# Optimization experiments

Measured on AMD Instinct MI355X. Metric: run time of the kernel, lower is better.

## Reference

```python
import jax, jax.numpy as jnp
import numpy as np

# ---- instant-NGP hash-grid config (matches module hparams) ----
L = 16              # num_levels
F = 2               # n_feats per level (hard-coded in lotd_auto_compute_cfg)
T = 2 ** 19         # log2_hashmap_size = 19
BASE, DESIRED = 16, 2048
N = 2097152         # ray samples per batch
GEO = 15            # geo_feat_dim
HID = 64            # layer_dim
APP_N, APP_D = 1000, 48
SH_DIM = 16         # degree-4 spherical harmonics

_b = np.exp(np.log(DESIRED / BASE) / (L - 1))
RES = jnp.asarray(np.floor(BASE * _b ** np.arange(L)).astype(np.float32))
OFFS = jnp.asarray(np.array([[(i >> 2) & 1, (i >> 1) & 1, i & 1] for i in range(8)]), jnp.uint32)
PRIMES = jnp.array([1, 2654435761, 805459861], dtype=jnp.uint32)


def hash_encode(x01, table):
    """x01: [N,3] in [0,1]; table: [L,T,F] -> [N, L*F] multi-res hash features."""
    def level(res, emb):
        xs = x01 * res                      # [N,3]
        x0 = jnp.floor(xs)
        w = xs - x0                         # trilinear weights
        c = x0.astype(jnp.uint32)[:, None, :] + OFFS[None]          # [N,8,3] corners
        h = c * PRIMES[None, None, :]       # uint32 wrap-around multiply
        idx = (h[..., 0] ^ h[..., 1] ^ h[..., 2]) & jnp.uint32(T - 1)  # [N,8] spatial hash
        f = emb[idx]                        # [N,8,F] gather
        ws = jnp.prod(jnp.where(OFFS[None] == 1, w[:, None, :], 1.0 - w[:, None, :]), axis=-1)
        return jnp.einsum('nc,ncf->nf', ws, f)
    feats = jax.vmap(level, in_axes=(0, 0), out_axes=1)(RES, table)  # [N,L,F]
    return feats.reshape(x01.shape[0], L * F)


def sh16(d):
    """degree-4 real spherical harmonics of unit dirs d: [N,3] -> [N,16]."""
    x, y, z = d[:, 0], d[:, 1], d[:, 2]
    xx, yy, zz = x * x, y * y, z * z
    xy, yz, xz = x * y, y * z, x * z
    return jnp.stack([
        0.28209479177387814 * jnp.ones_like(x),
        -0.48860251190291987 * y, 0.48860251190291987 * z, -0.48860251190291987 * x,
        1.0925484305920792 * xy, -1.0925484305920792 * yz,
        0.94617469575755997 * zz - 0.31539156525252005,
        -1.0925484305920792 * xz, 0.54627421529603959 * (xx - yy),
        -0.59004358992664352 * y * (3.0 * xx - yy),
        2.8906114426405538 * xy * z,
        -0.45704579946446572 * y * (4.0 * zz - xx - yy),
        0.37317633259011546 * z * (2.0 * zz - 3.0 * xx - 3.0 * yy),
        -0.45704579946446572 * x * (4.0 * zz - xx - yy),
        1.4453057213202769 * z * (xx - yy),
        -0.59004358992664352 * x * (xx - 3.0 * yy),
    ], axis=-1)


def setup_inputs() -> dict:
    key = jax.random.key(0)
    ks = jax.random.split(key, 16)
    def w(k, i, o):
        return jax.random.normal(k, (i, o), jnp.float32) / np.sqrt(i)
    x = jax.random.uniform(ks[0], (N, 3), jnp.float32, -1.0, 1.0)   # points in [-1,1]^3
    d = jax.random.normal(ks[1], (N, 3), jnp.float32)
    app_idx = jax.random.randint(ks[2], (N,), 0, APP_N, jnp.int32)
    hash_table = jax.random.uniform(ks[3], (L, T, F), jnp.float32, -1e-4, 1e-4)
    app_table = jax.random.normal(ks[4], (APP_N, APP_D), jnp.float32) * 0.05
    ci = GEO + SH_DIM + APP_D
    return {
        'x': x, 'd': d, 'app_idx': app_idx,
        'hash_table': hash_table, 'app_table': app_table,
        'sw0': w(ks[5], L * F, HID), 'sb0': jnp.zeros((HID,), jnp.float32),
        'sw1': w(ks[6], HID, 1 + GEO), 'sb1': jnp.zeros((1 + GEO,), jnp.float32),
        'cw0': w(ks[7], ci, HID), 'cb0': jnp.zeros((HID,), jnp.float32),
        'cw1': w(ks[8], HID, HID), 'cb1': jnp.zeros((HID,), jnp.float32),
        'cw2': w(ks[9], HID, 3), 'cb2': jnp.zeros((3,), jnp.float32),
    }


def reference(x, d, app_idx, hash_table, app_table,
              sw0, sb0, sw1, sb1, cw0, cb0, cw1, cb1, cw2, cb2):
    x01 = (x + 1.0) * 0.5                      # normalize to [0,1]^3
    enc = hash_encode(x01, hash_table)          # [N, 32]
    h = jax.nn.relu(enc @ sw0 + sb0)
    h = h @ sw1 + sb1                           # [N, 1+GEO]
    sigma = jax.nn.softplus(100.0 * h[:, :1]) / 100.0   # softplus(beta=100)
    geo = h[:, 1:]
    dn = d / jnp.linalg.norm(d, axis=-1, keepdims=True)
    sh = sh16(dn)                               # [N,16]
    a = app_table[app_idx]                      # [N,48] appearance embedding
    c = jnp.concatenate([geo, sh, a], axis=-1)
    c = jax.nn.relu(c @ cw0 + cb0)
    c = jax.nn.relu(c @ cw1 + cb1)
    rgb = jax.nn.sigmoid(c @ cw2 + cb2)         # [N,3]
    return jnp.concatenate([sigma, rgb], axis=-1)   # [N,4]
```

## Files before the change

### kernel.cpp

```cpp
#include <hip/hip_runtime.h>
#include <cmath>
#include <type_traits>

#define NL 16
#define TBL_N (1u << 19)
#define HID 64
#define NDL 6

typedef float f4v __attribute__((ext_vector_type(4)));
typedef float f2v __attribute__((ext_vector_type(2)));
typedef short s8v __attribute__((ext_vector_type(8)));
typedef unsigned int u32;
typedef unsigned short u16;

struct Res16 { float r[NL]; };
struct DenseP { int R[NDL]; int off[NDL]; int total; };

__device__ __host__ __forceinline__ unsigned short f2bf(float f) {
    unsigned u = __builtin_bit_cast(unsigned, f);
    unsigned r = (u + 0x7FFFu + ((u >> 16) & 1u)) >> 16;
    return (unsigned short)r;
}
__device__ __forceinline__ u32 pack_bf(float a, float b) {
    return (u32)f2bf(a) | ((u32)f2bf(b) << 16);
}
__device__ __forceinline__ void corner_vals(unsigned v, float& f0, float& f1) {
    f0 = __uint_as_float(v << 16);
    f1 = __uint_as_float(v & 0xffff0000u);
}
__device__ __forceinline__ void corner_vals(float2 v, float& f0, float& f1) {
    f0 = v.x; f1 = v.y;
}

__global__ __launch_bounds__(256) void repack_bf16(const float* __restrict__ src,
                                                   unsigned* __restrict__ dst, int n) {
    int i = blockIdx.x * blockDim.x + threadIdx.x;
    if (i >= n) return;
    f2v v = __builtin_nontemporal_load((const f2v*)src + i);
    dst[i] = pack_bf(v.x, v.y);
}

__global__ __launch_bounds__(256) void pos_prep(
    const float* __restrict__ x, f4v* __restrict__ pos, int p0, int P, int n_pts)
{
    int p = blockIdx.x * 256 + threadIdx.x;
    if (p >= P) return;
    int n = p0 + p;
    f4v v;
    v.x = (__builtin_nontemporal_load(&x[3*n+0]) + 1.f) * 0.5f;
    v.y = (__builtin_nontemporal_load(&x[3*n+1]) + 1.f) * 0.5f;
    v.z = (__builtin_nontemporal_load(&x[3*n+2]) + 1.f) * 0.5f;
    v.w = 0.f;
    pos[p] = v;
}

__global__ __launch_bounds__(256) void build_dense4(
    const u32* __restrict__ tbl, uint4* __restrict__ dense, DenseP dp)
{
    int e = blockIdx.x * 256 + threadIdx.x;
    if (e >= dp.total) return;
    int l = 0;
    #pragma unroll
    for (int i = 1; i < NDL; i++) if (e >= dp.off[i]) l = i;
    int cell = e - dp.off[l];
    int R = dp.R[l];
    int Z = cell % R; int t = cell / R; int Y = t % R; int X = t / R;
    u32 hy0 = (u32)Y * 2654435761u, hy1 = hy0 + 2654435761u;
    u32 hz0 = (u32)Z * 805459861u,  hz1 = hz0 + 805459861u;
    const u32* base = tbl + (size_t)l * TBL_N;
    uint4 v;
    v.x = base[((u32)X ^ hy0 ^ hz0) & (TBL_N - 1u)];
    v.y = base[((u32)X ^ hy0 ^ hz1) & (TBL_N - 1u)];
    v.z = base[((u32)X ^ hy1 ^ hz0) & (TBL_N - 1u)];
    v.w = base[((u32)X ^ hy1 ^ hz1) & (TBL_N - 1u)];
    dense[e] = v;
}

__global__ __launch_bounds__(256) void nerf_encode(
    const f4v* __restrict__ pos,
    const uint2* __restrict__ tbl2,
    const uint4* __restrict__ dense,
    u32* __restrict__ enc,
    Res16 rt, DenseP dp, int P)
{
    int l = blockIdx.y;
    int tid = threadIdx.x;
    int p = blockIdx.x * 256 + tid;
    int pc = min(p, P - 1);

    f4v pv = pos[pc];
    float px = pv.x, py = pv.y, pz = pv.z;

    float res = rt.r[l];
    float xs = px*res, ys = py*res, zs = pz*res;
    float fx = floorf(xs), fy = floorf(ys), fz = floorf(zs);
    float wx = xs - fx, wy = ys - fy, wz = zs - fz;
    float ax = 1.f - wx, ay = 1.f - wy, az = 1.f - wz;

    float e0 = 0.f, e1 = 0.f;
    if (l < NDL) {
        int R = dp.R[l];
        int X = (int)fx, Y = (int)fy, Z = (int)fz;
        const uint4* dl = dense + dp.off[l];
        int c00 = (X * R + Y) * R + Z;
        uint4 v0 = dl[c00];
        uint4 v1 = dl[c00 + R * R];
        float s00 = ay*az, s01 = ay*wz, s10 = wy*az, s11 = wy*wz;
        float f0, f1;
        corner_vals(v0.x, f0, f1); e0 += ax*s00*f0; e1 += ax*s00*f1;
        corner_vals(v0.y, f0, f1); e0 += ax*s01*f0; e1 += ax*s01*f1;
        corner_vals(v0.z, f0, f1); e0 += ax*s10*f0; e1 += ax*s10*f1;
        corner_vals(v0.w, f0, f1); e0 += ax*s11*f0; e1 += ax*s11*f1;
        corner_vals(v1.x, f0, f1); e0 += wx*s00*f0; e1 += wx*s00*f1;
        corner_vals(v1.y, f0, f1); e0 += wx*s01*f0; e1 += wx*s01*f1;
        corner_vals(v1.z, f0, f1); e0 += wx*s10*f0; e1 += wx*s10*f1;
        corner_vals(v1.w, f0, f1); e0 += wx*s11*f0; e1 += wx*s11*f1;
    } else {
        unsigned X = (unsigned)fx;
        unsigned Y = (unsigned)fy, Z = (unsigned)fz;
        unsigned hy0 = Y * 2654435761u, hy1 = hy0 + 2654435761u;
        unsigned hz0 = Z * 805459861u,  hz1 = hz0 + 805459861u;
        bool xodd = (X & 1u) != 0u;
        const uint2* b2 = tbl2 + (size_t)l * (TBL_N / 2);
        #pragma unroll
        for (int c = 0; c < 4; c++) {
            unsigned hyz = ((c & 2) ? hy1 : hy0) ^ ((c & 1) ? hz1 : hz0);
            float wyz = ((c & 2) ? wy : ay) * ((c & 1) ? wz : az);
            unsigned idxA = (X ^ hyz) & (TBL_N - 1u);
            uint2 vA = b2[idxA >> 1];
            u32 a = (idxA & 1u) ? vA.y : vA.x;
            u32 b = (idxA & 1u) ? vA.x : vA.y;
            if (xodd) {
                unsigned idxB = ((X + 1u) ^ hyz) & (TBL_N - 1u);
                uint2 vB = b2[idxB >> 1];
                b = (idxB & 1u) ? vB.y : vB.x;
            }
            float fa0, fa1, fb0, fb1;
            corner_vals(a, fa0, fa1);
            corner_vals(b, fb0, fb1);
            e0 += wyz * (ax * fa0 + wx * fb0);
            e1 += wyz * (ax * fa1 + wx * fb1);
        }
    }
    __builtin_nontemporal_store(pack_bf(e0, e1), &enc[(size_t)l * P + pc]);
}

__global__ __launch_bounds__(256) void nerf_pack_w(
    const float* __restrict__ sw0, const float* __restrict__ sb0,
    const float* __restrict__ sw1, const float* __restrict__ sb1,
    const float* __restrict__ cw0, const float* __restrict__ cb0,
    const float* __restrict__ cw1, const float* __restrict__ cb1,
    const float* __restrict__ cw2, const float* __restrict__ cb2,
    u16* __restrict__ wf, float* __restrict__ bi)
{
    int tid = threadIdx.x;
    for (int e = tid; e < 14336; e += 256) {
        int f = e >> 9, r = e & 511, lane = r >> 3, j = r & 7;
        int fo = lane & 15, G = lane >> 4;
        float val = 0.f;
        if (f < 4) {
            int o = f*16 + fo, i = G*8 + j;
            val = sw0[i*64 + o];
        } else if (f < 6) {
            int o = fo, i = (f-4)*32 + G*8 + j;
            val = sw1[i*16 + o];
        } else if (f < 18) {
            int t = f - 6, mt = t / 3, kt = t % 3;
            int o = mt*16 + fo, i = kt*32 + G*8 + j;
            int row = (i < 16) ? (15 + i) : (i < 64) ? (31 + (i - 16)) : (i < 79) ? (i - 64) : -1;
            val = (row < 0) ? 0.f : cw0[row*64 + o];
        } else if (f < 26) {
            int t = f - 18, mt = t >> 1, kt = t & 1;
            int o = mt*16 + fo, i = kt*32 + G*8 + j;
            val = cw1[i*64 + o];
        } else {
            int kt = f - 26;
            int o = fo, i = kt*32 + G*8 + j;
            val = (o < 3) ? cw2[i*3 + o] : 0.f;
        }
        wf[e] = f2bf(val);
    }
    for (int i2 = tid; i2 < 224; i2 += 256) {
        float v;
        if (i2 < 64) v = sb0[i2];
        else if (i2 < 80) v = sb1[i2 - 64];
        else if (i2 < 144) v = cb0[i2 - 80];
        else if (i2 < 208) v = cb1[i2 - 144];
        else v = (i2 - 208 < 3) ? cb2[i2 - 208] : 0.f;
        bi[i2] = v;
    }
}

#define ASTRIDE 104

__global__ __launch_bounds__(256) void nerf_mlp_mfma(
    const u16* __restrict__ wfg, const float* __restrict__ big,
    const u32* __restrict__ enc,
    const float* __restrict__ dvec, const int* __restrict__ app_idx,
    const float* __restrict__ app_table,
    float* __restrict__ out, int p0, int P, int n_pts)
{
    __shared__ __align__(16) u16 WF[14336];
    __shared__ __align__(16) float BI[224];
    __shared__ __align__(16) u16 ACT[4][16 * ASTRIDE];

    int tid = threadIdx.x;
    int w = tid >> 6, l = tid & 63;
    int G = l >> 4, pq = l & 15;

    for (int i = tid; i < 1792; i += 256) ((uint4*)WF)[i] = ((const uint4*)wfg)[i];
    for (int i = tid; i < 224; i += 256) BI[i] = big[i];
    if (G == 3) {
        ACT[w][pq*ASTRIDE + 79] = 0;
        #pragma unroll
        for (int k = 0; k < 8; k++) *(u32*)&ACT[w][pq*ASTRIDE + 80 + 2*k] = 0u;
    }
    __syncthreads();

    #pragma unroll 1
    for (int g = 0; g < 4; g++) {
        int pl = blockIdx.x * 256 + w * 64 + g * 16 + pq;
        int pc = min(pl, P - 1);
        int n = p0 + pc;

        uint4 ed;
        {
            const u32* encp = enc + pc;
            ed.x = __builtin_nontemporal_load(encp + (size_t)(4*G+0) * P);
            ed.y = __builtin_nontemporal_load(encp + (size_t)(4*G+1) * P);
            ed.z = __builtin_nontemporal_load(encp + (size_t)(4*G+2) * P);
            ed.w = __builtin_nontemporal_load(encp + (size_t)(4*G+3) * P);
        }
        s8v encf = __builtin_bit_cast(s8v, ed);
        float dx = __builtin_nontemporal_load(&dvec[3*n+0]);
        float dy = __builtin_nontemporal_load(&dvec[3*n+1]);
        float dz = __builtin_nontemporal_load(&dvec[3*n+2]);
        int ai = app_idx[n];
        const f4v* arow = (const f4v*)(app_table + (size_t)ai * 48 + 12 * G);
        f4v a0 = arow[0], a1 = arow[1], a2 = arow[2];

        f4v acc0[4];
        #pragma unroll
        for (int mt = 0; mt < 4; mt++) acc0[mt] = *(const f4v*)&BI[mt*16 + 4*G];
        #pragma unroll
        for (int mt = 0; mt < 4; mt++) {
            s8v wfr = *(const s8v*)&WF[mt*512 + l*8];
            acc0[mt] = __builtin_amdgcn_mfma_f32_16x16x32_bf16(wfr, encf, acc0[mt], 0, 0, 0);
        }
        #pragma unroll
        for (int mt = 0; mt < 4; mt++) {
            f4v v = acc0[mt];
            *(u32*)&ACT[w][pq*ASTRIDE + mt*16 + 4*G]     = pack_bf(fmaxf(v[0],0.f), fmaxf(v[1],0.f));
            *(u32*)&ACT[w][pq*ASTRIDE + mt*16 + 4*G + 2] = pack_bf(fmaxf(v[2],0.f), fmaxf(v[3],0.f));
        }

        f4v acc1 = *(const f4v*)&BI[64 + 4*G];
        #pragma unroll
        for (int kt = 0; kt < 2; kt++) {
            s8v b = *(const s8v*)&ACT[w][pq*ASTRIDE + kt*32 + G*8];
            s8v wfr = *(const s8v*)&WF[(4+kt)*512 + l*8];
            acc1 = __builtin_amdgcn_mfma_f32_16x16x32_bf16(wfr, b, acc1, 0, 0, 0);
        }
        float sig_raw = acc1[0];

        {
            float invn = 1.0f / sqrtf(dx*dx + dy*dy + dz*dz);
            float ndx = dx*invn, ndy = dy*invn, ndz = dz*invn;
            float xx = ndx*ndx, yy = ndy*ndy, zz = ndz*ndz;
            float xy = ndx*ndy, yz = ndy*ndz, xz = ndx*ndz;
            float s0, s1, s2, s3;
            if (G == 0) {
                s0 =  0.28209479177387814f;
                s1 = -0.48860251190291987f * ndy;
                s2 =  0.48860251190291987f * ndz;
                s3 = -0.48860251190291987f * ndx;
            } else if (G == 1) {
                s0 =  1.0925484305920792f * xy;
                s1 = -1.0925484305920792f * yz;
                s2 =  0.94617469575756f * zz - 0.31539156525252005f;
                s3 = -1.0925484305920792f * xz;
            } else if (G == 2) {
                s0 =  0.5462742152960396f * (xx - yy);
                s1 = -0.5900435899266435f * ndy * (3.f*xx - yy);
                s2 =  2.890611442640554f * xy * ndz;
                s3 = -0.4570457994644657f * ndy * (4.f*zz - xx - yy);
            } else {
                s0 =  0.37317633259011546f * ndz * (2.f*zz - 3.f*xx - 3.f*yy);
                s1 = -0.4570457994644657f * ndx * (4.f*zz - xx - yy);
                s2 =  1.445305721320277f * ndz * (xx - yy);
                s3 = -0.5900435899266435f * ndx * (xx - 3.f*yy);
            }
            *(u32*)&ACT[w][pq*ASTRIDE + 4*G]     = pack_bf(s0, s1);
            *(u32*)&ACT[w][pq*ASTRIDE + 4*G + 2] = pack_bf(s2, s3);
            *(u32*)&ACT[w][pq*ASTRIDE + 16 + 12*G     ] = pack_bf(a0[0], a0[1]);
            *(u32*)&ACT[w][pq*ASTRIDE + 16 + 12*G + 2 ] = pack_bf(a0[2], a0[3]);
            *(u32*)&ACT[w][pq*ASTRIDE + 16 + 12*G + 4 ] = pack_bf(a1[0], a1[1]);
            *(u32*)&ACT[w][pq*ASTRIDE + 16 + 12*G + 6 ] = pack_bf(a1[2], a1[3]);
            *(u32*)&ACT[w][pq*ASTRIDE + 16 + 12*G + 8 ] = pack_bf(a2[0], a2[1]);
            *(u32*)&ACT[w][pq*ASTRIDE + 16 + 12*G + 10] = pack_bf(a2[2], a2[3]);
            #pragma unroll
            for (int r2 = 0; r2 < 4; r2++) {
                int fp = 4*G + r2;
                if (fp >= 1) ACT[w][pq*ASTRIDE + 63 + fp] = f2bf(acc1[r2]);
            }
        }

        f4v acc[4];
        #pragma unroll
        for (int mt = 0; mt < 4; mt++) acc[mt] = *(const f4v*)&BI[80 + mt*16 + 4*G];
        #pragma unroll
        for (int kt = 0; kt < 3; kt++) {
            s8v b = *(const s8v*)&ACT[w][pq*ASTRIDE + kt*32 + G*8];
            #pragma unroll
            for (int mt = 0; mt < 4; mt++) {
                s8v wfr = *(const s8v*)&WF[(6 + mt*3 + kt)*512 + l*8];
                acc[mt] = __builtin_amdgcn_mfma_f32_16x16x32_bf16(wfr, b, acc[mt], 0, 0, 0);
            }
        }
        #pragma unroll
        for (int mt = 0; mt < 4; mt++) {
            f4v v = acc[mt];
            *(u32*)&ACT[w][pq*ASTRIDE + mt*16 + 4*G]     = pack_bf(fmaxf(v[0],0.f), fmaxf(v[1],0.f));
            *(u32*)&ACT[w][pq*ASTRIDE + mt*16 + 4*G + 2] = pack_bf(fmaxf(v[2],0.f), fmaxf(v[3],0.f));
        }

        #pragma unroll
        for (int mt = 0; mt < 4; mt++) acc[mt] = *(const f4v*)&BI[144 + mt*16 + 4*G];
        #pragma unroll
        for (int kt = 0; kt < 2; kt++) {
            s8v b = *(const s8v*)&ACT[w][pq*ASTRIDE + kt*32 + G*8];
            #pragma unroll
            for (int mt = 0; mt < 4; mt++) {
                s8v wfr = *(const s8v*)&WF[(18 + mt*2 + kt)*512 + l*8];
                acc[mt] = __builtin_amdgcn_mfma_f32_16x16x32_bf16(wfr, b, acc[mt], 0, 0, 0);
            }
        }
        #pragma unroll
        for (int mt = 0; mt < 4; mt++) {
            f4v v = acc[mt];
            *(u32*)&ACT[w][pq*ASTRIDE + mt*16 + 4*G]     = pack_bf(fmaxf(v[0],0.f), fmaxf(v[1],0.f));
            *(u32*)&ACT[w][pq*ASTRIDE + mt*16 + 4*G + 2] = pack_bf(fmaxf(v[2],0.f), fmaxf(v[3],0.f));
        }

        f4v acc2 = *(const f4v*)&BI[208 + 4*G];
        #pragma unroll
        for (int kt = 0; kt < 2; kt++) {
            s8v b = *(const s8v*)&ACT[w][pq*ASTRIDE + kt*32 + G*8];
            s8v wfr = *(const s8v*)&WF[(26+kt)*512 + l*8];
            acc2 = __builtin_amdgcn_mfma_f32_16x16x32_bf16(wfr, b, acc2, 0, 0, 0);
        }

        if (G == 0 && pl < P) {
            float z100 = 100.f * sig_raw;
            float sigma = (z100 > 20.f) ? sig_raw : (log1pf(expf(z100)) * 0.01f);
            f4v o4;
            o4[0] = sigma;
            o4[1] = 1.f/(1.f+expf(-acc2[0]));
            o4[2] = 1.f/(1.f+expf(-acc2[1]));
            o4[3] = 1.f/(1.f+expf(-acc2[2]));
            __builtin_nontemporal_store(o4, (f4v*)out + (size_t)(p0 + pl));
        }
    }
}

template <int USE_BF16>
__global__ __launch_bounds__(256) void nerf_fused(
    const float* __restrict__ x,
    const float* __restrict__ dvec,
    const int*   __restrict__ app_idx,
    const void*  __restrict__ tbl_raw,
    const float* __restrict__ app_table,
    const float* __restrict__ sw0, const float* __restrict__ sb0,
    const float* __restrict__ sw1, const float* __restrict__ sb1,
    const float* __restrict__ cw0, const float* __restrict__ cb0,
    const float* __restrict__ cw1, const float* __restrict__ cb1,
    const float* __restrict__ cw2, const float* __restrict__ cb2,
    float* __restrict__ out, Res16 rt, int n_pts)
{
    using CT = typename std::conditional<USE_BF16 != 0, unsigned, float2>::type;
    const CT* __restrict__ tbl = (const CT*)tbl_raw;

    int n = blockIdx.x * blockDim.x + threadIdx.x;
    if (n >= n_pts) return;

    float px = (x[3*n+0] + 1.f) * 0.5f;
    float py = (x[3*n+1] + 1.f) * 0.5f;
    float pz = (x[3*n+2] + 1.f) * 0.5f;

    float e[2*NL];
    #pragma unroll
    for (int l = 0; l < NL; l++) {
        float res = rt.r[l];
        float xs = px*res, ys = py*res, zs = pz*res;
        float fx = floorf(xs), fy = floorf(ys), fz = floorf(zs);
        float wx = xs - fx, wy = ys - fy, wz = zs - fz;
        float ax = 1.f - wx, ay = 1.f - wy, az = 1.f - wz;
        unsigned X = (unsigned)fx, Y = (unsigned)fy, Z = (unsigned)fz;
        unsigned hx0 = X,               hx1 = X + 1u;
        unsigned hy0 = Y * 2654435761u, hy1 = hy0 + 2654435761u;
        unsigned hz0 = Z * 805459861u,  hz1 = hz0 + 805459861u;
        const CT* base = tbl + (size_t)l * TBL_N;
        float e0 = 0.f, e1 = 0.f;
        #pragma unroll
        for (int c = 0; c < 8; c++) {
            unsigned idx = (((c & 4) ? hx1 : hx0) ^
                            ((c & 2) ? hy1 : hy0) ^
                            ((c & 1) ? hz1 : hz0)) & (TBL_N - 1u);
            CT v = base[idx];
            float f0, f1;
            corner_vals(v, f0, f1);
            float wgt = ((c & 4) ? wx : ax) * ((c & 2) ? wy : ay) * ((c & 1) ? wz : az);
            e0 += wgt * f0;
            e1 += wgt * f1;
        }
        e[2*l] = e0; e[2*l+1] = e1;
    }

    float h[HID];
    #pragma unroll
    for (int o = 0; o < HID; o++) h[o] = sb0[o];
    #pragma unroll
    for (int l = 0; l < NL; l++) {
        const float* r0 = sw0 + (2 * l) * HID;
        float e0 = e[2*l], e1 = e[2*l+1];
        #pragma unroll
        for (int o = 0; o < HID; o++) h[o] += e0 * r0[o] + e1 * r0[HID + o];
    }
    #pragma unroll
    for (int o = 0; o < HID; o++) h[o] = fmaxf(h[o], 0.f);

    float h1[16];
    #pragma unroll
    for (int o = 0; o < 16; o++) h1[o] = sb1[o];
    #pragma unroll
    for (int i = 0; i < HID; i++) {
        float v = h[i];
        const float* wr = sw1 + i * 16;
        #pragma unroll
        for (int o = 0; o < 16; o++) h1[o] += v * wr[o];
    }

    float z100 = 100.f * h1[0];
    float sigma = (z100 > 20.f) ? h1[0] : (log1pf(expf(z100)) * 0.01f);

    float dx = dvec[3*n+0], dy = dvec[3*n+1], dz = dvec[3*n+2];
    float invn = 1.0f / sqrtf(dx*dx + dy*dy + dz*dz);
    dx *= invn; dy *= invn; dz *= invn;
    float xx = dx*dx, yy = dy*dy, zz = dz*dz;
    float xy = dx*dy, yz = dy*dz, xz = dx*dz;
    float sh[16];
    sh[0]  = 0.28209479177387814f;
    sh[1]  = -0.48860251190291987f * dy;
    sh[2]  =  0.48860251190291987f * dz;
    sh[3]  = -0.48860251190291987f * dx;
    sh[4]  =  1.0925484305920792f * xy;
    sh[5]  = -1.0925484305920792f * yz;
    sh[6]  =  0.94617469575756f * zz - 0.31539156525252005f;
    sh[7]  = -1.0925484305920792f * xz;
    sh[8]  =  0.5462742152960396f * (xx - yy);
    sh[9]  = -0.5900435899266435f * dy * (3.f * xx - yy);
    sh[10] =  2.890611442640554f * xy * dz;
    sh[11] = -0.4570457994644657f * dy * (4.f * zz - xx - yy);
    sh[12] =  0.37317633259011546f * dz * (2.f * zz - 3.f * xx - 3.f * yy);
    sh[13] = -0.4570457994644657f * dx * (4.f * zz - xx - yy);
    sh[14] =  1.445305721320277f * dz * (xx - yy);
    sh[15] = -0.5900435899266435f * dx * (xx - 3.f * yy);

    float c1[HID];
    #pragma unroll
    for (int o = 0; o < HID; o++) c1[o] = cb0[o];
    #pragma unroll
    for (int i = 0; i < 15; i++) {
        float v = h1[i + 1];
        const float* wr = cw0 + i * HID;
        #pragma unroll
        for (int o = 0; o < HID; o++) c1[o] += v * wr[o];
    }
    #pragma unroll
    for (int i = 0; i < 16; i++) {
        float v = sh[i];
        const float* wr = cw0 + (15 + i) * HID;
        #pragma unroll
        for (int o = 0; o < HID; o++) c1[o] += v * wr[o];
    }
    {
        const float4* arow = reinterpret_cast<const float4*>(app_table + (size_t)app_idx[n] * 48);
        for (int j4 = 0; j4 < 12; j4++) {
            float4 v = arow[j4];
            const float* wr = cw0 + (31 + 4 * j4) * HID;
            #pragma unroll
            for (int o = 0; o < HID; o++) c1[o] += v.x * wr[o];
            #pragma unroll
            for (int o = 0; o < HID; o++) c1[o] += v.y * wr[HID + o];
            #pragma unroll
            for (int o = 0; o < HID; o++) c1[o] += v.z * wr[2 * HID + o];
            #pragma unroll
            for (int o = 0; o < HID; o++) c1[o] += v.w * wr[3 * HID + o];
        }
    }
    #pragma unroll
    for (int o = 0; o < HID; o++) c1[o] = fmaxf(c1[o], 0.f);

    float c2[HID];
    #pragma unroll
    for (int o = 0; o < HID; o++) c2[o] = cb1[o];
    #pragma unroll
    for (int i = 0; i < HID; i++) {
        float v = c1[i];
        const float* wr = cw1 + i * HID;
        #pragma unroll
        for (int o = 0; o < HID; o++) c2[o] += v * wr[o];
    }
    #pragma unroll
    for (int o = 0; o < HID; o++) c2[o] = fmaxf(c2[o], 0.f);

    float r = cb2[0], g = cb2[1], b = cb2[2];
    #pragma unroll
    for (int i = 0; i < HID; i++) {
        float v = c2[i];
        r += v * cw2[i * 3 + 0];
        g += v * cw2[i * 3 + 1];
        b += v * cw2[i * 3 + 2];
    }
    r = 1.f / (1.f + expf(-r));
    g = 1.f / (1.f + expf(-g));
    b = 1.f / (1.f + expf(-b));

    reinterpret_cast<float4*>(out)[n] = make_float4(sigma, r, g, b);
}

extern "C" void kernel_launch(void* const* d_in, const int* in_sizes, int n_in,
                              void* d_out, int out_size, void* d_ws, size_t ws_size,
                              hipStream_t stream) {
    const float* x         = (const float*)d_in[0];
    const float* dvec      = (const float*)d_in[1];
    const int*   app_idx   = (const int*)  d_in[2];
    const float* ht        = (const float*)d_in[3];
    const float* app_table = (const float*)d_in[4];
    const float* sw0 = (const float*)d_in[5];
    const float* sb0 = (const float*)d_in[6];
    const float* sw1 = (const float*)d_in[7];
    const float* sb1 = (const float*)d_in[8];
    const float* cw0 = (const float*)d_in[9];
    const float* cb0 = (const float*)d_in[10];
    const float* cw1 = (const float*)d_in[11];
    const float* cb1 = (const float*)d_in[12];
    const float* cw2 = (const float*)d_in[13];
    const float* cb2 = (const float*)d_in[14];

    int n_pts = in_sizes[0] / 3;

    Res16 rt;
    double bb = exp(log(2048.0 / 16.0) / 15.0);
    for (int l = 0; l < NL; l++) rt.r[l] = (float)floor(16.0 * pow(bb, (double)l));

    DenseP dp;
    {
        int acc = 0;
        for (int l = 0; l < NDL; l++) {
            dp.R[l] = (int)rt.r[l] + 1;
            dp.off[l] = acc;
            acc += dp.R[l] * dp.R[l] * dp.R[l];
        }
        dp.total = acc;
    }

    const size_t tbl_entries = (size_t)NL * TBL_N;
    const size_t tbl_bytes = tbl_entries * sizeof(unsigned);
    const size_t WFRAG_OFF = tbl_bytes;
    const size_t BIAS_OFF  = WFRAG_OFF + 14336 * 2;
    const size_t DENSE_OFF = (BIAS_OFF + 224 * 4 + 255) & ~(size_t)255;
    const size_t CHUNK_OFF = (DENSE_OFF + (size_t)dp.total * 16 + 255) & ~(size_t)255;

    if (ws_size >= CHUNK_OFF + (8u << 20)) {
        int nent = (int)tbl_entries;
        hipLaunchKernelGGL(repack_bf16, dim3((nent + 255) / 256), dim3(256), 0, stream,
                           ht, (unsigned*)d_ws, nent);
        u16*   wfrag = (u16*)  ((char*)d_ws + WFRAG_OFF);
        float* biasb = (float*)((char*)d_ws + BIAS_OFF);
        uint4* dense = (uint4*)((char*)d_ws + DENSE_OFF);
        hipLaunchKernelGGL(nerf_pack_w, dim3(1), dim3(256), 0, stream,
                           sw0, sb0, sw1, sb1, cw0, cb0, cw1, cb1, cw2, cb2,
                           wfrag, biasb);
        hipLaunchKernelGGL(build_dense4, dim3((dp.total + 255) / 256), dim3(256), 0, stream,
                           (const u32*)d_ws, dense, dp);

        size_t cap = (ws_size - CHUNK_OFF) / 80;
        if (cap > (size_t)n_pts) cap = (size_t)n_pts;
        cap &= ~(size_t)255;
        if (cap == 0) cap = 256;
        f4v* pos = (f4v*)((char*)d_ws + CHUNK_OFF);
        u32* enc = (u32*)((char*)d_ws + CHUNK_OFF + cap * 16);

        for (long p0 = 0; p0 < (long)n_pts; p0 += (long)cap) {
            int P = (int)(((long)n_pts - p0) < (long)cap ? ((long)n_pts - p0) : (long)cap);
            hipLaunchKernelGGL(pos_prep, dim3((P + 255) / 256), dim3(256), 0, stream,
                               x, pos, (int)p0, P, n_pts);
            hipLaunchKernelGGL(nerf_encode, dim3((P + 255) / 256, NL), dim3(256), 0, stream,
                               pos, (const uint2*)d_ws, dense, enc, rt, dp, P);
            hipLaunchKernelGGL(nerf_mlp_mfma, dim3((P + 255) / 256), dim3(256), 0, stream,
                               wfrag, biasb, enc,
                               dvec, app_idx, app_table,
                               (float*)d_out, (int)p0, P, n_pts);
        }
    } else if (ws_size >= tbl_bytes) {
        int nent = (int)tbl_entries;
        hipLaunchKernelGGL(repack_bf16, dim3((nent + 255) / 256), dim3(256), 0, stream,
                           ht, (unsigned*)d_ws, nent);
        dim3 g((n_pts + 255) / 256), blk(256);
        hipLaunchKernelGGL((nerf_fused<1>), g, blk, 0, stream,
                           x, dvec, app_idx, (const void*)d_ws, app_table,
                           sw0, sb0, sw1, sb1, cw0, cb0, cw1, cb1, cw2, cb2,
                           (float*)d_out, rt, n_pts);
    } else {
        dim3 g((n_pts + 255) / 256), blk(256);
        hipLaunchKernelGGL((nerf_fused<0>), g, blk, 0, stream,
                           x, dvec, app_idx, (const void*)ht, app_table,
                           sw0, sb0, sw1, sb1, cw0, cb0, cw1, cb1, cw2, cb2,
                           (float*)d_out, rt, n_pts);
    }
}
```

Before: 916.1 us.

## Use 16-byte hash-table fetches for x-neighbor corners and hold MLP weights in registers

In the hashed levels of the encode kernel, each corner fetch now loads a 16-byte group of four bf16 entries. It takes the x+1 neighbor from the same load whenever both hash indices fall in the same group, and issues a second load only otherwise. This is meant to cut gather transactions over the old scheme, which used 8-byte pairs and paired entries only in some cases. The MLP kernel drops its shared-memory weight buffer and keeps all 28 bf16 MFMA weight fragments in registers per lane. That removes the LDS loads before each MFMA but adds about 112 VGPRs per lane, which can reduce occupancy.

Measured after the change: 784.7 us, median of 2. 1.17x faster.

```diff
diff --git a/kernel.cpp b/kernel.cpp
--- a/kernel.cpp
+++ b/kernel.cpp
@@ -28,8 +28,10 @@
     f0 = __uint_as_float(v << 16);
     f1 = __uint_as_float(v & 0xffff0000u);
 }
-__device__ __forceinline__ void corner_vals(float2 v, float& f0, float& f1) {
-    f0 = v.x; f1 = v.y;
+__device__ __forceinline__ u32 sel4(uint4 v, unsigned i) {
+    u32 lo = (i & 1u) ? v.y : v.x;
+    u32 hi = (i & 1u) ? v.w : v.z;
+    return (i & 2u) ? hi : lo;
 }
 
 __global__ __launch_bounds__(256) void repack_bf16(const float* __restrict__ src,
@@ -78,7 +80,7 @@
 
 __global__ __launch_bounds__(256) void nerf_encode(
     const f4v* __restrict__ pos,
-    const uint2* __restrict__ tbl2,
+    const uint4* __restrict__ tbl4,
     const uint4* __restrict__ dense,
     u32* __restrict__ enc,
     Res16 rt, DenseP dp, int P)
@@ -116,24 +118,25 @@
         corner_vals(v1.z, f0, f1); e0 += wx*s10*f0; e1 += wx*s10*f1;
         corner_vals(v1.w, f0, f1); e0 += wx*s11*f0; e1 += wx*s11*f1;
     } else {
-        unsigned X = (unsigned)fx;
+        unsigned X = (unsigned)fx, Xp = X + 1u;
         unsigned Y = (unsigned)fy, Z = (unsigned)fz;
         unsigned hy0 = Y * 2654435761u, hy1 = hy0 + 2654435761u;
         unsigned hz0 = Z * 805459861u,  hz1 = hz0 + 805459861u;
-        bool xodd = (X & 1u) != 0u;
-        const uint2* b2 = tbl2 + (size_t)l * (TBL_N / 2);
+        const uint4* b4 = tbl4 + (size_t)l * (TBL_N / 4);
         #pragma unroll
         for (int c = 0; c < 4; c++) {
             unsigned hyz = ((c & 2) ? hy1 : hy0) ^ ((c & 1) ? hz1 : hz0);
             float wyz = ((c & 2) ? wy : ay) * ((c & 1) ? wz : az);
-            unsigned idxA = (X ^ hyz) & (TBL_N - 1u);
-            uint2 vA = b2[idxA >> 1];
-            u32 a = (idxA & 1u) ? vA.y : vA.x;
-            u32 b = (idxA & 1u) ? vA.x : vA.y;
-            if (xodd) {
-                unsigned idxB = ((X + 1u) ^ hyz) & (TBL_N - 1u);
-                uint2 vB = b2[idxB >> 1];
-                b = (idxB & 1u) ? vB.y : vB.x;
+            unsigned idxA = (X  ^ hyz) & (TBL_N - 1u);
+            unsigned idxB = (Xp ^ hyz) & (TBL_N - 1u);
+            uint4 vA = b4[idxA >> 2];
+            u32 a = sel4(vA, idxA & 3u);
+            u32 b;
+            if ((idxB >> 2) == (idxA >> 2)) {
+                b = sel4(vA, idxB & 3u);
+            } else {
+                uint4 vB = b4[idxB >> 2];
+                b = sel4(vB, idxB & 3u);
             }
             float fa0, fa1, fb0, fb1;
             corner_vals(a, fa0, fa1);
@@ -200,7 +203,6 @@
     const float* __restrict__ app_table,
     float* __restrict__ out, int p0, int P, int n_pts)
 {
-    __shared__ __align__(16) u16 WF[14336];
     __shared__ __align__(16) float BI[224];
     __shared__ __align__(16) u16 ACT[4][16 * ASTRIDE];
 
@@ -208,7 +210,11 @@
     int w = tid >> 6, l = tid & 63;
     int G = l >> 4, pq = l & 15;
 
-    for (int i = tid; i < 1792; i += 256) ((uint4*)WF)[i] = ((const uint4*)wfg)[i];
+    s8v wreg[28];
+    #pragma unroll
+    for (int f = 0; f < 28; f++)
+        wreg[f] = *(const s8v*)(wfg + f * 512 + l * 8);
+
     for (int i = tid; i < 224; i += 256) BI[i] = big[i];
     if (G == 3) {
         ACT[w][pq*ASTRIDE + 79] = 0;
@@ -243,10 +249,8 @@
         #pragma unroll
         for (int mt = 0; mt < 4; mt++) acc0[mt] = *(const f4v*)&BI[mt*16 + 4*G];
         #pragma unroll
-        for (int mt = 0; mt < 4; mt++) {
-            s8v wfr = *(const s8v*)&WF[mt*512 + l*8];
-            acc0[mt] = __builtin_amdgcn_mfma_f32_16x16x32_bf16(wfr, encf, acc0[mt], 0, 0, 0);
-        }
+        for (int mt = 0; mt < 4; mt++)
+            acc0[mt] = __builtin_amdgcn_mfma_f32_16x16x32_bf16(wreg[mt], encf, acc0[mt], 0, 0, 0);
         #pragma unroll
         for (int mt = 0; mt < 4; mt++) {
             f4v v = acc0[mt];
@@ -258,8 +262,7 @@
         #pragma unroll
         for (int kt = 0; kt < 2; kt++) {
             s8v b = *(const s8v*)&ACT[w][pq*ASTRIDE + kt*32 + G*8];
-            s8v wfr = *(const s8v*)&WF[(4+kt)*512 + l*8];
-            acc1 = __builtin_amdgcn_mfma_f32_16x16x32_bf16(wfr, b, acc1, 0, 0, 0);
+            acc1 = __builtin_amdgcn_mfma_f32_16x16x32_bf16(wreg[4+kt], b, acc1, 0, 0, 0);
         }
         float sig_raw = acc1[0];
 
@@ -312,10 +315,8 @@
         for (int kt = 0; kt < 3; kt++) {
             s8v b = *(const s8v*)&ACT[w][pq*ASTRIDE + kt*32 + G*8];
             #pragma unroll
-            for (int mt = 0; mt < 4; mt++) {
-                s8v wfr = *(const s8v*)&WF[(6 + mt*3 + kt)*512 + l*8];
-                acc[mt] = __builtin_amdgcn_mfma_f32_16x16x32_bf16(wfr, b, acc[mt], 0, 0, 0);
-            }
+            for (int mt = 0; mt < 4; mt++)
+                acc[mt] = __builtin_amdgcn_mfma_f32_16x16x32_bf16(wreg[6 + mt*3 + kt], b, acc[mt], 0, 0, 0);
         }
         #pragma unroll
         for (int mt = 0; mt < 4; mt++) {
@@ -330,10 +331,8 @@
         for (int kt = 0; kt < 2; kt++) {
             s8v b = *(const s8v*)&ACT[w][pq*ASTRIDE + kt*32 + G*8];
             #pragma unroll
-            for (int mt = 0; mt < 4; mt++) {
-                s8v wfr = *(const s8v*)&WF[(18 + mt*2 + kt)*512 + l*8];
-                acc[mt] = __builtin_amdgcn_mfma_f32_16x16x32_bf16(wfr, b, acc[mt], 0, 0, 0);
-            }
+            for (int mt = 0; mt < 4; mt++)
+                acc[mt] = __builtin_amdgcn_mfma_f32_16x16x32_bf16(wreg[18 + mt*2 + kt], b, acc[mt], 0, 0, 0);
         }
         #pragma unroll
         for (int mt = 0; mt < 4; mt++) {
@@ -346,8 +345,7 @@
         #pragma unroll
         for (int kt = 0; kt < 2; kt++) {
             s8v b = *(const s8v*)&ACT[w][pq*ASTRIDE + kt*32 + G*8];
-            s8v wfr = *(const s8v*)&WF[(26+kt)*512 + l*8];
-            acc2 = __builtin_amdgcn_mfma_f32_16x16x32_bf16(wfr, b, acc2, 0, 0, 0);
+            acc2 = __builtin_amdgcn_mfma_f32_16x16x32_bf16(wreg[26+kt], b, acc2, 0, 0, 0);
         }
 
         if (G == 0 && pl < P) {
@@ -408,7 +406,8 @@
                             ((c & 1) ? hz1 : hz0)) & (TBL_N - 1u);
             CT v = base[idx];
             float f0, f1;
-            corner_vals(v, f0, f1);
+            if constexpr (USE_BF16 != 0) { corner_vals((unsigned)v, f0, f1); }
+            else { float2 vv = *(float2*)&v; f0 = vv.x; f1 = vv.y; }
             float wgt = ((c & 4) ? wx : ax) * ((c & 2) ? wy : ay) * ((c & 1) ? wz : az);
             e0 += wgt * f0;
             e1 += wgt * f1;
@@ -597,7 +596,7 @@
             hipLaunchKernelGGL(pos_prep, dim3((P + 255) / 256), dim3(256), 0, stream,
                                x, pos, (int)p0, P, n_pts);
             hipLaunchKernelGGL(nerf_encode, dim3((P + 255) / 256, NL), dim3(256), 0, stream,
-                               pos, (const uint2*)d_ws, dense, enc, rt, dp, P);
+                               pos, (const uint4*)d_ws, dense, enc, rt, dp, P);
             hipLaunchKernelGGL(nerf_mlp_mfma, dim3((P + 255) / 256), dim3(256), 0, stream,
                                wfrag, biasb, enc,
                                dvec, app_idx, app_table,
```
